# Kernel optimization log

Hardware: AMD Instinct MI355X
Metric: run time of the kernel (lower is better)

Reference implementation:

```python
import jax, jax.numpy as jnp
import numpy as np

GRID_SIZE = 8
POS_LAMBDA = 1.0
POS_MARGIN = 1.0
NEG_MARGIN = 0.2
LOSS_LAMBDA = 1.0

N, C, HR, WR = 4, 256, 60, 60
H, W = HR * GRID_SIZE, WR * GRID_SIZE


def setup_inputs() -> dict:
    key = jax.random.key(0)
    k1, k2, k3 = jax.random.split(key, 3)
    desc1 = jax.random.normal(k1, (N, C, HR, WR), dtype=jnp.float32)
    desc2 = jax.random.normal(k2, (N, C, HR, WR), dtype=jnp.float32)
    # near-identity homographies to keep the perspective divide well-conditioned
    noise = jax.random.normal(k3, (N, 3, 3), dtype=jnp.float32) * 0.01
    homo21 = jnp.eye(3, dtype=jnp.float32)[None] + noise
    vis_mask1 = jnp.ones((N, 1, H, W), dtype=jnp.float32)
    return {"desc1": desc1, "desc2": desc2, "homo21": homo21, "vis_mask1": vis_mask1}


def reference(desc1, desc2, homo21, vis_mask1):
    n, c, hr, wr = desc1.shape
    gs = GRID_SIZE
    dt = desc1.dtype
    # cell-center coordinate grid, (x, y) order: hr x wr x 2
    ys, xs = jnp.meshgrid(jnp.arange(hr, dtype=dt), jnp.arange(wr, dtype=dt), indexing="ij")
    grid = jnp.stack([xs, ys], axis=-1) * gs + gs // 2
    grid = jnp.broadcast_to(grid[None], (n, hr, wr, 2))
    # warp grid by homography: n x hr x wr x 2
    pts = jnp.concatenate([grid, jnp.ones((n, hr, wr, 1), dtype=dt)], axis=-1)
    wpts = jnp.einsum("nij,nhwj->nhwi", homo21, pts)
    w_grid = wpts[..., :2] / wpts[..., 2:3]
    # all-pairs distance between grid (dims 1,2) and warped grid (dims 3,4)
    diff = grid[:, :, :, None, None, :] - w_grid[:, None, None, :, :, :]
    grid_dist = jnp.linalg.norm(diff, axis=-1)  # n,hr,wr,hr,wr
    s = (grid_dist <= gs - 0.5).astype(dt)
    ns = 1.0 - s
    # space_to_depth(vis_mask1, gs).prod(dim=1): product over each gs x gs block
    vm = vis_mask1[:, 0].reshape(n, hr, gs, wr, gs).prod(axis=(2, 4))  # n,hr,wr
    vm = vm.reshape(n, 1, 1, hr, wr)
    s = s * vm
    ns = ns * vm
    # all-pairs descriptor dot product: n,hr,wr,hr,wr
    dot_desc = jnp.einsum("nchw,ncij->nhwij", desc1, desc2)
    pos_dist = jnp.maximum(POS_MARGIN - dot_desc, 0.0)
    neg_dist = jnp.maximum(dot_desc - NEG_MARGIN, 0.0)
    loss = POS_LAMBDA * s * pos_dist + ns * neg_dist
    norm = hr * wr * vm.sum()
    return loss.sum() / norm * LOSS_LAMBDA
```

## Files before the change

### kernel.cpp

```cpp
#include <hip/hip_runtime.h>
#include <stdint.h>

#define NB   4
#define CC   256
#define WR   60
#define MM   3600
#define HH   480
#define WW   480
#define GS   8
#define MT   29
#define NBLK (MT * MT * NB)
#define PREPB 57

typedef float f32x4 __attribute__((ext_vector_type(4)));
typedef long  l64x2 __attribute__((ext_vector_type(2)));

__global__ __launch_bounds__(256) void pack_prep(
    const float* __restrict__ d1, const float* __restrict__ d2,
    const float* __restrict__ homo, const float* __restrict__ vis,
    unsigned char* __restrict__ p1, unsigned char* __restrict__ p2,
    float2* __restrict__ wg, float* __restrict__ vmarr,
    float* __restrict__ vm_part) {
  __shared__ float vmred[4];
  int kt = blockIdx.x, mtile = blockIdx.y, z = blockIdx.z;
  int bid = kt + 8 * (mtile + MT * z);
  int b = z & 3;
  const float* src = ((z >> 2) ? d2 : d1) + (size_t)b * CC * MM + (size_t)(kt * 32) * MM;
  unsigned char* dst = ((z >> 2) ? p2 : p1) + ((size_t)(b * MT + mtile) * 8 + kt) * 4096;
  int tid = threadIdx.x;
  int lane = tid & 63, pp = (tid >> 6) & 1, h = tid >> 7;
  int r = lane & 15;
  int k0 = (lane >> 4) * 8;

  unsigned ww[4];
#pragma unroll
  for (int j = 0; j < 2; ++j) {
    int gm = mtile * 128 + h * 64 + (2 * pp + j) * 16 + r;
    unsigned w01 = 0, w23 = 0;
    if (gm < MM) {
      const float* s0 = src + (size_t)k0 * MM + gm;
      float f0 = s0[0 * MM], f1 = s0[1 * MM], f2 = s0[2 * MM], f3 = s0[3 * MM];
      float f4 = s0[4 * MM], f5 = s0[5 * MM], f6 = s0[6 * MM], f7 = s0[7 * MM];
      w01 = __builtin_amdgcn_cvt_pk_fp8_f32(f0, f1, 0, false);
      w01 = __builtin_amdgcn_cvt_pk_fp8_f32(f2, f3, w01, true);
      w23 = __builtin_amdgcn_cvt_pk_fp8_f32(f4, f5, 0, false);
      w23 = __builtin_amdgcn_cvt_pk_fp8_f32(f6, f7, w23, true);
    }
    ww[2 * j]     = w01;
    ww[2 * j + 1] = w23;
  }
  uint4 o; o.x = ww[0]; o.y = ww[1]; o.z = ww[2]; o.w = ww[3];
  ((uint4*)dst)[tid] = o;

  if (bid < PREPB) {
    int idx = bid * 256 + tid;
    float p = 0.f;
    if (idx < NB * MM) {
      int bb = idx / MM, cell = idx - bb * MM;
      int h1 = cell / WR, w1 = cell - h1 * WR;
      float gx = (float)(w1 * GS + GS / 2);
      float gy = (float)(h1 * GS + GS / 2);
      const float* Hm = homo + bb * 9;
      float X = Hm[0] * gx + Hm[1] * gy + Hm[2];
      float Y = Hm[3] * gx + Hm[4] * gy + Hm[5];
      float Z = Hm[6] * gx + Hm[7] * gy + Hm[8];
      wg[idx] = make_float2(X / Z, Y / Z);
      const float* v = vis + (size_t)bb * HH * WW + (size_t)(h1 * GS) * WW + w1 * GS;
      float prod = 1.f;
#pragma unroll
      for (int rr = 0; rr < GS; ++rr) {
        const float4* rp = (const float4*)(v + (size_t)rr * WW);
        float4 a = rp[0], c = rp[1];
        prod *= a.x * a.y * a.z * a.w;
        prod *= c.x * c.y * c.z * c.w;
      }
      vmarr[idx] = prod;
      p = prod;
    }
#pragma unroll
    for (int off = 32; off; off >>= 1) p += __shfl_down(p, off, 64);
    if ((tid & 63) == 0) vmred[tid >> 6] = p;
    __syncthreads();
    if (tid == 0)
      vm_part[bid] = vmred[0] + vmred[1] + vmred[2] + vmred[3];
  }
}

__global__ __launch_bounds__(256, 4) void hinge_gemm(
    const unsigned char* __restrict__ Ap, const unsigned char* __restrict__ Bp,
    const float2* __restrict__ wg, const float* __restrict__ vmarr,
    float* __restrict__ block_part) {
  __shared__ float partial[4];

  int b = blockIdx.z, mtile = blockIdx.y, ntile = blockIdx.x;
  int tid = threadIdx.x, lane = tid & 63, w = tid >> 6;
  int quad = lane >> 4, r = lane & 15;
  int wave_m = w >> 1, wave_n = w & 1;

  const char* Af = (const char*)Ap + ((size_t)(b * MT + mtile) * 8) * 4096
                   + wave_m * 2048 + lane * 16;
  const char* Bf = (const char*)Bp + ((size_t)(b * MT + ntile) * 8) * 4096
                   + wave_n * 2048 + lane * 16;

  f32x4 acc[4][4];
#pragma unroll
  for (int i = 0; i < 4; ++i)
#pragma unroll
    for (int j = 0; j < 4; ++j)
#pragma unroll
      for (int k = 0; k < 4; ++k) acc[i][j][k] = 0.f;

  long a0[4], b0[4], a1[4], b1[4];
#pragma unroll
  for (int p = 0; p < 2; ++p) {
    l64x2 va = *(const l64x2*)(Af + p * 1024);
    l64x2 vb = *(const l64x2*)(Bf + p * 1024);
    a0[2 * p] = va.x; a0[2 * p + 1] = va.y;
    b0[2 * p] = vb.x; b0[2 * p + 1] = vb.y;
  }

#pragma unroll
  for (int kt = 0; kt < 8; ++kt) {
    if (kt < 7) {
      const char* an = Af + (kt + 1) * 4096;
      const char* bn = Bf + (kt + 1) * 4096;
#pragma unroll
      for (int p = 0; p < 2; ++p) {
        l64x2 va = *(const l64x2*)(an + p * 1024);
        l64x2 vb = *(const l64x2*)(bn + p * 1024);
        a1[2 * p] = va.x; a1[2 * p + 1] = va.y;
        b1[2 * p] = vb.x; b1[2 * p + 1] = vb.y;
      }
    }
#pragma unroll
    for (int mt = 0; mt < 4; ++mt)
#pragma unroll
      for (int nt = 0; nt < 4; ++nt)
        acc[mt][nt] = __builtin_amdgcn_mfma_f32_16x16x32_fp8_fp8(
            a0[mt], b0[nt], acc[mt][nt], 0, 0, 0);
#pragma unroll
    for (int t = 0; t < 4; ++t) { a0[t] = a1[t]; b0[t] = b1[t]; }
  }

  float gxv[16], gyv[16];
#pragma unroll
  for (int mt = 0; mt < 4; ++mt)
#pragma unroll
    for (int reg = 0; reg < 4; ++reg) {
      int gm = mtile * 128 + wave_m * 64 + mt * 16 + quad * 4 + reg;
      float gmf = (float)gm;
      float h1 = floorf(fmaf(gmf, (1.0f / 60.0f), (1.0f / 120.0f)));
      float w1 = fmaf(h1, -60.f, gmf);
      gxv[mt * 4 + reg] = fmaf(w1, 8.f, 4.f);
      gyv[mt * 4 + reg] = fmaf(h1, 8.f, 4.f);
    }

  float sum = 0.f;
  const float2* wgb = wg + (size_t)b * MM;
  const float*  vmb = vmarr + (size_t)b * MM;
#pragma unroll
  for (int nt = 0; nt < 4; ++nt) {
    int gn = ntile * 128 + wave_n * 64 + nt * 16 + r;
    bool nok = gn < MM;
    float2 wgv = nok ? wgb[gn] : make_float2(1e9f, 1e9f);
    float  vmv = nok ? vmb[gn] : 0.f;
#pragma unroll
    for (int mt = 0; mt < 4; ++mt)
#pragma unroll
      for (int reg = 0; reg < 4; ++reg) {
        float dot = acc[mt][nt][reg];
        float dx = gxv[mt * 4 + reg] - wgv.x;
        float dy = gyv[mt * 4 + reg] - wgv.y;
        float d2 = fmaf(dx, dx, dy * dy);
        float a = (d2 <= 56.25f) ? (1.0f - dot) : (dot - 0.2f);
        sum = fmaf(vmv, fmaxf(a, 0.f), sum);
      }
  }
#pragma unroll
  for (int off = 32; off; off >>= 1) sum += __shfl_down(sum, off, 64);
  if (lane == 0) partial[w] = sum;
  __syncthreads();
  if (tid == 0) {
    int fbid = ntile + MT * (mtile + MT * b);
    block_part[fbid] = partial[0] + partial[1] + partial[2] + partial[3];
  }
}

__global__ __launch_bounds__(256) void finalize_k(
    const float* __restrict__ block_part, const float* __restrict__ vm_part,
    float* __restrict__ out) {
  __shared__ float red[8];
  int tid = threadIdx.x;
  float s = 0.f, v = 0.f;
  for (int i = tid; i < NBLK; i += 256) s += block_part[i];
  if (tid < PREPB) v = vm_part[tid];
#pragma unroll
  for (int off = 32; off; off >>= 1) {
    s += __shfl_down(s, off, 64);
    v += __shfl_down(v, off, 64);
  }
  if ((tid & 63) == 0) { red[tid >> 6] = s; red[4 + (tid >> 6)] = v; }
  __syncthreads();
  if (tid == 0) {
    float S = red[0] + red[1] + red[2] + red[3];
    float V = red[4] + red[5] + red[6] + red[7];
    out[0] = S / ((float)MM * V);
  }
}

extern "C" void kernel_launch(void* const* d_in, const int* in_sizes, int n_in,
                              void* d_out, int out_size, void* d_ws, size_t ws_size,
                              hipStream_t stream) {
  const float* desc1 = (const float*)d_in[0];
  const float* desc2 = (const float*)d_in[1];
  const float* homo  = (const float*)d_in[2];
  const float* vis   = (const float*)d_in[3];
  float* out = (float*)d_out;

  char* ws = (char*)d_ws;
  unsigned char* Ap = (unsigned char*)ws;
  unsigned char* Bp = (unsigned char*)(ws + 3801088);
  float2* wg         = (float2*)(ws + 7602176);
  float*  vm         = (float*) (ws + 7717376);
  float*  vm_part    = (float*) (ws + 7774976);
  float*  block_part = (float*) (ws + 7775232);

  dim3 pgrid(8, MT, 2 * NB);
  pack_prep<<<pgrid, 256, 0, stream>>>(desc1, desc2, homo, vis, Ap, Bp,
                                       wg, vm, vm_part);

  dim3 ggrid(MT, MT, NB);
  hinge_gemm<<<ggrid, 256, 0, stream>>>(Ap, Bp, wg, vm, block_part);

  finalize_k<<<1, 256, 0, stream>>>(block_part, vm_part, out);
}
```

Measured before the change: 116.9 us.

## Switch GEMM to 32x32x64 scaled FP8 MFMA with repacked layout and XCD remap

Replaces the 16x16x32 FP8 MFMA with the gfx950 scaled 32x32x64 f8f6f4 MFMA, using unit scales. The pack kernel is rewritten to emit a matching 32-byte-per-lane operand layout, and the pack grid is halved along K. The GEMM block index is also remapped so that neighbouring tiles land on the same XCD for L2 reuse, and launch bounds drop to 2 blocks per CU. The goal is fewer MFMA issues and larger operand loads, at the cost of more registers and possibly lower occupancy.

```diff
diff --git a/kernel.cpp b/kernel.cpp
--- a/kernel.cpp
+++ b/kernel.cpp
@@ -12,8 +12,9 @@
 #define NBLK (MT * MT * NB)
 #define PREPB 57
 
-typedef float f32x4 __attribute__((ext_vector_type(4)));
-typedef long  l64x2 __attribute__((ext_vector_type(2)));
+typedef float f32x4  __attribute__((ext_vector_type(4)));
+typedef float f32x16 __attribute__((ext_vector_type(16)));
+typedef int   i32x8  __attribute__((ext_vector_type(8)));
 
 __global__ __launch_bounds__(256) void pack_prep(
     const float* __restrict__ d1, const float* __restrict__ d2,
@@ -22,35 +23,39 @@
     float2* __restrict__ wg, float* __restrict__ vmarr,
     float* __restrict__ vm_part) {
   __shared__ float vmred[4];
-  int kt = blockIdx.x, mtile = blockIdx.y, z = blockIdx.z;
-  int bid = kt + 8 * (mtile + MT * z);
+  int kt = blockIdx.x;
+  int mtile = blockIdx.y;
+  int z = blockIdx.z;
+  int bid = kt + 4 * (mtile + MT * z);
   int b = z & 3;
-  const float* src = ((z >> 2) ? d2 : d1) + (size_t)b * CC * MM + (size_t)(kt * 32) * MM;
-  unsigned char* dst = ((z >> 2) ? p2 : p1) + ((size_t)(b * MT + mtile) * 8 + kt) * 4096;
+  const float* src = ((z >> 2) ? d2 : d1) + (size_t)b * CC * MM;
+  unsigned char* dstbase = ((z >> 2) ? p2 : p1) + (size_t)(b * MT + mtile) * 32768;
   int tid = threadIdx.x;
-  int lane = tid & 63, pp = (tid >> 6) & 1, h = tid >> 7;
-  int r = lane & 15;
-  int k0 = (lane >> 4) * 8;
-
-  unsigned ww[4];
-#pragma unroll
-  for (int j = 0; j < 2; ++j) {
-    int gm = mtile * 128 + h * 64 + (2 * pp + j) * 16 + r;
-    unsigned w01 = 0, w23 = 0;
-    if (gm < MM) {
-      const float* s0 = src + (size_t)k0 * MM + gm;
-      float f0 = s0[0 * MM], f1 = s0[1 * MM], f2 = s0[2 * MM], f3 = s0[3 * MM];
-      float f4 = s0[4 * MM], f5 = s0[5 * MM], f6 = s0[6 * MM], f7 = s0[7 * MM];
-      w01 = __builtin_amdgcn_cvt_pk_fp8_f32(f0, f1, 0, false);
-      w01 = __builtin_amdgcn_cvt_pk_fp8_f32(f2, f3, w01, true);
-      w23 = __builtin_amdgcn_cvt_pk_fp8_f32(f4, f5, 0, false);
-      w23 = __builtin_amdgcn_cvt_pk_fp8_f32(f6, f7, w23, true);
-    }
-    ww[2 * j]     = w01;
-    ww[2 * j + 1] = w23;
-  }
-  uint4 o; o.x = ww[0]; o.y = ww[1]; o.z = ww[2]; o.w = ww[3];
-  ((uint4*)dst)[tid] = o;
+  int t = tid >> 6, lane = tid & 63;
+  int r = lane & 31, hi = lane >> 5;
+  int m = mtile * 128 + t * 32 + r;
+  int c0 = kt * 64 + hi * 32;
+
+  unsigned int ww[8];
+  if (m < MM) {
+    const float* s0 = src + (size_t)c0 * MM + m;
+#pragma unroll
+    for (int d = 0; d < 8; ++d) {
+      float f0 = s0[(size_t)(4 * d + 0) * MM];
+      float f1 = s0[(size_t)(4 * d + 1) * MM];
+      float f2 = s0[(size_t)(4 * d + 2) * MM];
+      float f3 = s0[(size_t)(4 * d + 3) * MM];
+      unsigned int wv = __builtin_amdgcn_cvt_pk_fp8_f32(f0, f1, 0, false);
+      wv = __builtin_amdgcn_cvt_pk_fp8_f32(f2, f3, wv, true);
+      ww[d] = wv;
+    }
+  } else {
+#pragma unroll
+    for (int d = 0; d < 8; ++d) ww[d] = 0;
+  }
+  uint4* dst = (uint4*)(dstbase + (size_t)(kt * 4 + t) * 2048 + lane * 32);
+  dst[0] = make_uint4(ww[0], ww[1], ww[2], ww[3]);
+  dst[1] = make_uint4(ww[4], ww[5], ww[6], ww[7]);
 
   if (bid < PREPB) {
     int idx = bid * 256 + tid;
@@ -86,91 +91,96 @@
   }
 }
 
-__global__ __launch_bounds__(256, 4) void hinge_gemm(
+__global__ __launch_bounds__(256, 2) void hinge_gemm(
     const unsigned char* __restrict__ Ap, const unsigned char* __restrict__ Bp,
     const float2* __restrict__ wg, const float* __restrict__ vmarr,
     float* __restrict__ block_part) {
   __shared__ float partial[4];
 
-  int b = blockIdx.z, mtile = blockIdx.y, ntile = blockIdx.x;
+  int orig = blockIdx.x + MT * blockIdx.y + MT * MT * blockIdx.z;
+  const int q = NBLK >> 3, rmod = NBLK & 7;
+  int xcd = orig & 7, loc = orig >> 3;
+  int wgid = (xcd < rmod ? xcd * (q + 1) : rmod * (q + 1) + (xcd - rmod) * q) + loc;
+  int b = wgid / (MT * MT);
+  int rem = wgid - b * (MT * MT);
+  int mtile = rem / MT;
+  int ntile = rem - mtile * MT;
+
   int tid = threadIdx.x, lane = tid & 63, w = tid >> 6;
-  int quad = lane >> 4, r = lane & 15;
+  int colL = lane & 31, hi = lane >> 5;
   int wave_m = w >> 1, wave_n = w & 1;
 
-  const char* Af = (const char*)Ap + ((size_t)(b * MT + mtile) * 8) * 4096
-                   + wave_m * 2048 + lane * 16;
-  const char* Bf = (const char*)Bp + ((size_t)(b * MT + ntile) * 8) * 4096
-                   + wave_n * 2048 + lane * 16;
-
-  f32x4 acc[4][4];
-#pragma unroll
-  for (int i = 0; i < 4; ++i)
-#pragma unroll
-    for (int j = 0; j < 4; ++j)
-#pragma unroll
-      for (int k = 0; k < 4; ++k) acc[i][j][k] = 0.f;
-
-  long a0[4], b0[4], a1[4], b1[4];
-#pragma unroll
-  for (int p = 0; p < 2; ++p) {
-    l64x2 va = *(const l64x2*)(Af + p * 1024);
-    l64x2 vb = *(const l64x2*)(Bf + p * 1024);
-    a0[2 * p] = va.x; a0[2 * p + 1] = va.y;
-    b0[2 * p] = vb.x; b0[2 * p + 1] = vb.y;
-  }
-
-#pragma unroll
-  for (int kt = 0; kt < 8; ++kt) {
-    if (kt < 7) {
-      const char* an = Af + (kt + 1) * 4096;
-      const char* bn = Bf + (kt + 1) * 4096;
-#pragma unroll
-      for (int p = 0; p < 2; ++p) {
-        l64x2 va = *(const l64x2*)(an + p * 1024);
-        l64x2 vb = *(const l64x2*)(bn + p * 1024);
-        a1[2 * p] = va.x; a1[2 * p + 1] = va.y;
-        b1[2 * p] = vb.x; b1[2 * p + 1] = vb.y;
+  const char* Af = (const char*)Ap + (size_t)(b * MT + mtile) * 32768
+                   + (size_t)(wave_m * 2) * 2048 + lane * 32;
+  const char* Bf = (const char*)Bp + (size_t)(b * MT + ntile) * 32768
+                   + (size_t)(wave_n * 2) * 2048 + lane * 32;
+
+  f32x16 acc[2][2];
+#pragma unroll
+  for (int i = 0; i < 2; ++i)
+#pragma unroll
+    for (int j = 0; j < 2; ++j)
+#pragma unroll
+      for (int k = 0; k < 16; ++k) acc[i][j][k] = 0.f;
+
+  i32x8 a0[2], b0[2], a1[2], b1[2];
+#pragma unroll
+  for (int t2 = 0; t2 < 2; ++t2) {
+    a0[t2] = *(const i32x8*)(Af + t2 * 2048);
+    b0[t2] = *(const i32x8*)(Bf + t2 * 2048);
+  }
+
+#pragma unroll
+  for (int kt = 0; kt < 4; ++kt) {
+    if (kt < 3) {
+      const char* an = Af + (kt + 1) * 8192;
+      const char* bn = Bf + (kt + 1) * 8192;
+#pragma unroll
+      for (int t2 = 0; t2 < 2; ++t2) {
+        a1[t2] = *(const i32x8*)(an + t2 * 2048);
+        b1[t2] = *(const i32x8*)(bn + t2 * 2048);
       }
     }
 #pragma unroll
-    for (int mt = 0; mt < 4; ++mt)
-#pragma unroll
-      for (int nt = 0; nt < 4; ++nt)
-        acc[mt][nt] = __builtin_amdgcn_mfma_f32_16x16x32_fp8_fp8(
-            a0[mt], b0[nt], acc[mt][nt], 0, 0, 0);
-#pragma unroll
-    for (int t = 0; t < 4; ++t) { a0[t] = a1[t]; b0[t] = b1[t]; }
-  }
-
-  float gxv[16], gyv[16];
-#pragma unroll
-  for (int mt = 0; mt < 4; ++mt)
-#pragma unroll
-    for (int reg = 0; reg < 4; ++reg) {
-      int gm = mtile * 128 + wave_m * 64 + mt * 16 + quad * 4 + reg;
+    for (int mi = 0; mi < 2; ++mi)
+#pragma unroll
+      for (int ni = 0; ni < 2; ++ni)
+        acc[mi][ni] = __builtin_amdgcn_mfma_scale_f32_32x32x64_f8f6f4(
+            a0[mi], b0[ni], acc[mi][ni], 0, 0,
+            0, 127, 0, 127 );
+#pragma unroll
+    for (int t2 = 0; t2 < 2; ++t2) { a0[t2] = a1[t2]; b0[t2] = b1[t2]; }
+  }
+
+  float gxv[32], gyv[32];
+#pragma unroll
+  for (int mi = 0; mi < 2; ++mi)
+#pragma unroll
+    for (int reg = 0; reg < 16; ++reg) {
+      int gm = mtile * 128 + wave_m * 64 + mi * 32 + (reg & 3) + 8 * (reg >> 2) + 4 * hi;
       float gmf = (float)gm;
       float h1 = floorf(fmaf(gmf, (1.0f / 60.0f), (1.0f / 120.0f)));
       float w1 = fmaf(h1, -60.f, gmf);
-      gxv[mt * 4 + reg] = fmaf(w1, 8.f, 4.f);
-      gyv[mt * 4 + reg] = fmaf(h1, 8.f, 4.f);
+      gxv[mi * 16 + reg] = fmaf(w1, 8.f, 4.f);
+      gyv[mi * 16 + reg] = fmaf(h1, 8.f, 4.f);
     }
 
   float sum = 0.f;
   const float2* wgb = wg + (size_t)b * MM;
   const float*  vmb = vmarr + (size_t)b * MM;
 #pragma unroll
-  for (int nt = 0; nt < 4; ++nt) {
-    int gn = ntile * 128 + wave_n * 64 + nt * 16 + r;
+  for (int ni = 0; ni < 2; ++ni) {
+    int gn = ntile * 128 + wave_n * 64 + ni * 32 + colL;
     bool nok = gn < MM;
     float2 wgv = nok ? wgb[gn] : make_float2(1e9f, 1e9f);
     float  vmv = nok ? vmb[gn] : 0.f;
 #pragma unroll
-    for (int mt = 0; mt < 4; ++mt)
-#pragma unroll
-      for (int reg = 0; reg < 4; ++reg) {
-        float dot = acc[mt][nt][reg];
-        float dx = gxv[mt * 4 + reg] - wgv.x;
-        float dy = gyv[mt * 4 + reg] - wgv.y;
+    for (int mi = 0; mi < 2; ++mi)
+#pragma unroll
+      for (int reg = 0; reg < 16; ++reg) {
+        float dot = acc[mi][ni][reg];
+        float dx = gxv[mi * 16 + reg] - wgv.x;
+        float dy = gyv[mi * 16 + reg] - wgv.y;
         float d2 = fmaf(dx, dx, dy * dy);
         float a = (d2 <= 56.25f) ? (1.0f - dot) : (dot - 0.2f);
         sum = fmaf(vmv, fmaxf(a, 0.f), sum);
@@ -225,7 +235,7 @@
   float*  vm_part    = (float*) (ws + 7774976);
   float*  block_part = (float*) (ws + 7775232);
 
-  dim3 pgrid(8, MT, 2 * NB);
+  dim3 pgrid(4, MT, 2 * NB);
   pack_prep<<<pgrid, 256, 0, stream>>>(desc1, desc2, homo, vis, Ap, Bp,
                                        wg, vm, vm_part);
 
```

After: 114.6 us, median of 2. 2.0% less time.
